# Kernel tuning notes

Measured on AMD Instinct MI355X. Metric: run time of the kernel, lower is better.

Reference implementation:

```python
import jax, jax.numpy as jnp
import numpy as np

N, H = 8192, 1024

def setup_inputs() -> dict:
    key = jax.random.key(0)
    ks = jax.random.split(key, 7)
    s = 1.0 / np.sqrt(H)
    return {
        "x": jax.random.normal(ks[0], (N, H), dtype=jnp.float32),
        "Wq": jax.random.uniform(ks[1], (H, H), dtype=jnp.float32, minval=-s, maxval=s),
        "bq": jax.random.uniform(ks[2], (H,), dtype=jnp.float32, minval=-s, maxval=s),
        "Wk": jax.random.uniform(ks[3], (H, H), dtype=jnp.float32, minval=-s, maxval=s),
        "bk": jax.random.uniform(ks[4], (H,), dtype=jnp.float32, minval=-s, maxval=s),
        "Wv": jax.random.uniform(ks[5], (H, H), dtype=jnp.float32, minval=-s, maxval=s),
        "bv": jax.random.uniform(ks[6], (H,), dtype=jnp.float32, minval=-s, maxval=s),
    }

def reference(x, Wq, bq, Wk, bk, Wv, bv):
    # q/k/v projections: [N, H]
    q = x @ Wq + bq
    k = x @ Wk + bk
    v = x @ Wv + bv
    # full scores [N, N]; NOTE: original has no 1/sqrt(d) scaling
    scores = q @ k.T
    alpha = jax.nn.softmax(scores, axis=1)
    return alpha @ v
```

## Files before the change

### kernel.cpp

```cpp
#include <hip/hip_runtime.h>
#include <hip/hip_bf16.h>
#include <hip/hip_fp16.h>


typedef _Float16 f16x8 __attribute__((ext_vector_type(8)));
typedef float floatx4 __attribute__((ext_vector_type(4)));
typedef float floatx2 __attribute__((ext_vector_type(2)));
typedef unsigned short ushortx8 __attribute__((ext_vector_type(8)));

__device__ __forceinline__ unsigned short f2h(float f) {
  __half h = __float2half(f);
  return __builtin_bit_cast(unsigned short, h);
}
__device__ __forceinline__ float h2f(unsigned short u) {
  return __half2float(__builtin_bit_cast(__half, u));
}

__device__ __forceinline__ void async16(const void* g, void* l) {
  __builtin_amdgcn_global_load_lds(
      (__attribute__((address_space(1))) unsigned int*)(g),
      (__attribute__((address_space(3))) unsigned int*)(l),
      16, 0, 0);
}


__global__ __launch_bounds__(256) void conv_f32_f16(const float* __restrict__ in,
                                                    unsigned short* __restrict__ out,
                                                    long n) {
  long i = ((long)blockIdx.x * 256 + threadIdx.x) * 4;
  if (i + 3 < n) {
    float4 f = *(const float4*)(in + i);
    ushort4 o;
    o.x = f2h(f.x); o.y = f2h(f.y); o.z = f2h(f.z); o.w = f2h(f.w);
    *(ushort4*)(out + i) = o;
  }
}

__global__ __launch_bounds__(256) void transpose_f32_f16_3(const float* __restrict__ in0,
                                                           const float* __restrict__ in1,
                                                           const float* __restrict__ in2,
                                                           unsigned short* __restrict__ out,
                                                           int rows, int cols) {
  const float* in = (blockIdx.z == 0) ? in0 : (blockIdx.z == 1) ? in1 : in2;
  unsigned short* o = out + (size_t)blockIdx.z * rows * cols;
  __shared__ float tile[32][33];
  int bx = blockIdx.x * 32;
  int by = blockIdx.y * 32;
  int tx = threadIdx.x & 31, ty = threadIdx.x >> 5;
  #pragma unroll
  for (int yy = ty; yy < 32; yy += 8)
    tile[yy][tx] = in[(size_t)(by + yy) * cols + bx + tx];
  __syncthreads();
  #pragma unroll
  for (int yy = ty; yy < 32; yy += 8)
    o[(size_t)(bx + yy) * rows + by + tx] = f2h(tile[tx][yy]);
}

template <int MODE>
__global__ __launch_bounds__(256, 4)
void gemm_bt(const unsigned short* __restrict__ A,
             const unsigned short* __restrict__ B,
             int M, int Nn, int K,
             const float* __restrict__ b0, const float* __restrict__ b1,
             const float* __restrict__ b2,
             unsigned short* __restrict__ out) {
  if constexpr (MODE == 0) {
    B   += (size_t)blockIdx.z * Nn * K;
    out += (size_t)blockIdx.z * M * Nn;
  }
  const float* bias = (MODE != 0) ? nullptr
                      : (blockIdx.z == 0) ? b0 : (blockIdx.z == 1) ? b1 : b2;
  __shared__ unsigned short smem[128 * 136];
  unsigned short* As = smem;
  unsigned short* Bs = smem + 128 * 32;
  const int tid  = threadIdx.x;
  const int wave = tid >> 6;
  const int lane = tid & 63;
  const int wm = wave >> 1, wn = wave & 1;
  const int quad = lane >> 4, l16 = lane & 15;
  const long bm = (long)blockIdx.y * 128;
  const long bn = (long)blockIdx.x * 128;

  floatx4 acc[4][4] = {};

  const int srow = wave * 32 + (lane >> 2);
  const int scol = (lane & 3) * 8;
  const unsigned short* gA0 = A + (bm + srow) * (long)K + scol;
  const unsigned short* gA1 = gA0 + 16L * K;
  const unsigned short* gB0 = B + (bn + srow) * (long)K + scol;
  const unsigned short* gB1 = gB0 + 16L * K;
  unsigned short* lA0 = &As[(wave * 32) * 32];
  unsigned short* lA1 = &As[(wave * 32 + 16) * 32];
  unsigned short* lB0 = &Bs[(wave * 32) * 32];
  unsigned short* lB1 = &Bs[(wave * 32 + 16) * 32];

  for (int kk = 0; kk < K; kk += 32) {
    async16(gA0 + kk, lA0);
    async16(gA1 + kk, lA1);
    async16(gB0 + kk, lB0);
    async16(gB1 + kk, lB1);
    __syncthreads();
    f16x8 af[4], bfv[4];
    #pragma unroll
    for (int i = 0; i < 4; ++i) {
      af[i]  = *reinterpret_cast<const f16x8*>(&As[(wm * 64 + i * 16 + l16) * 32 + quad * 8]);
      bfv[i] = *reinterpret_cast<const f16x8*>(&Bs[(wn * 64 + i * 16 + l16) * 32 + quad * 8]);
    }
    #pragma unroll
    for (int i = 0; i < 4; ++i)
      #pragma unroll
      for (int j = 0; j < 4; ++j)
        acc[i][j] = __builtin_amdgcn_mfma_f32_16x16x32_f16(af[i], bfv[j], acc[i][j], 0, 0, 0);
    __syncthreads();
  }
  #pragma unroll
  for (int i = 0; i < 4; ++i) {
    const int row0 = wm * 64 + i * 16 + quad * 4;
    #pragma unroll
    for (int j = 0; j < 4; ++j) {
      const int col = wn * 64 + j * 16 + l16;
      const float cb = (MODE == 0) ? bias[bn + col] : 0.0f;
      #pragma unroll
      for (int r = 0; r < 4; ++r)
        smem[(row0 + r) * 136 + col] = f2h(acc[i][j][r] + cb);
    }
  }
  __syncthreads();
  #pragma unroll
  for (int u = 0; u < 8; ++u) {
    const int chunk = u * 256 + tid;
    const int row = chunk >> 4;
    const int cc = chunk & 15;
    const ushortx8 val = *reinterpret_cast<const ushortx8*>(&smem[row * 136 + cc * 8]);
    *reinterpret_cast<ushortx8*>(&out[(bm + row) * (long)Nn + bn + cc * 8]) = val;
  }
}

__global__ __launch_bounds__(256) void softmax_compact(unsigned short* __restrict__ S,
                                                       int* __restrict__ nnz, int n) {
  const int row = blockIdx.x;
  const int tid = threadIdx.x;
  const int lane = tid & 63, w = tid >> 6;
  unsigned short* prow = S + (size_t)row * n;

  float v[32];
  float m = -1e30f;
  #pragma unroll
  for (int u = 0; u < 4; ++u) {
    const ushortx8 c = *reinterpret_cast<const ushortx8*>(&prow[tid * 32 + u * 8]);
    #pragma unroll
    for (int e = 0; e < 8; ++e) {
      v[u * 8 + e] = h2f(c[e]);
      m = fmaxf(m, v[u * 8 + e]);
    }
  }
  #pragma unroll
  for (int off = 32; off > 0; off >>= 1) m = fmaxf(m, __shfl_down(m, off, 64));
  __shared__ float redm[4];
  __shared__ int cnt;
  if (lane == 0) redm[w] = m;
  if (tid == 0) cnt = 0;
  __syncthreads();
  m = fmaxf(fmaxf(redm[0], redm[1]), fmaxf(redm[2], redm[3]));

  float s = 0.0f;
  #pragma unroll
  for (int i = 0; i < 32; ++i) {
    v[i] = __expf(v[i] - m);
    s += v[i];
  }
  #pragma unroll
  for (int off = 32; off > 0; off >>= 1) s += __shfl_down(s, off, 64);
  __shared__ float reds[4];
  if (lane == 0) reds[w] = s;
  __syncthreads();
  s = reds[0] + reds[1] + reds[2] + reds[3];
  const float inv = 1.0f / s;

  unsigned int* pairs = (unsigned int*)prow;
  const int cap = n / 2;
  #pragma unroll
  for (int i = 0; i < 32; ++i) {
    unsigned short hh = f2h(v[i] * inv);
    if (hh) {
      int p = atomicAdd(&cnt, 1);
      if (p < cap) pairs[p] = ((unsigned int)(tid * 32 + i) << 16) | hh;
    }
  }
  __syncthreads();
  const int c = (cnt < cap) ? cnt : cap;
  const int padded = (c + 7) & ~7;
  if (tid < padded - c) pairs[c + tid] = 0u;
  if (tid == 0) nnz[row] = padded;
}

__global__ __launch_bounds__(256) void pv_sliced(const unsigned short* __restrict__ S,
                                                 const int* __restrict__ nnz,
                                                 const unsigned short* __restrict__ v,
                                                 float* __restrict__ out,
                                                 int n) {
  const int wave = threadIdx.x >> 6;
  const int lane = threadIdx.x & 63;
  const int colbase = blockIdx.x * 128 + lane * 2;
  const unsigned colbyte = (unsigned)colbase * 2;
  const char* __restrict__ vb = (const char*)v;
  const char* __restrict__ sb = (const char*)S;

  #pragma unroll 1
  for (int r = 0; r < 4; ++r) {
    const int row = blockIdx.y + ((wave << 2) + r) * 512;
    int craw = nnz[row];
    craw = craw < 0 ? 0 : (craw > 4096 ? 4096 : craw);
    const int cnt = __builtin_amdgcn_readfirstlane(craw);
    const unsigned rowbase = (unsigned)row << 14;
    const unsigned pend = rowbase + 16384 - 32;
    unsigned poff = rowbase;
    uint4 q0 = *(const uint4*)(sb + poff);
    uint4 q1 = *(const uint4*)(sb + poff + 16);
    float a0 = 0.f, a1 = 0.f;
    for (int j = 0; j < cnt; j += 8) {
      const unsigned pn = (poff + 32 <= pend) ? poff + 32 : pend;
      const uint4 n0 = *(const uint4*)(sb + pn);
      const uint4 n1 = *(const uint4*)(sb + pn + 16);
      const unsigned p[8] = {q0.x, q0.y, q0.z, q0.w, q1.x, q1.y, q1.z, q1.w};
      #pragma unroll
      for (int u = 0; u < 8; ++u) {
        const ushort2 vv = *(const ushort2*)(vb + (((p[u] & 0xffff0000u) >> 5) + colbyte));
        const float w = h2f((unsigned short)(p[u] & 0xffffu));
        a0 += w * h2f(vv.x);
        a1 += w * h2f(vv.y);
      }
      q0 = n0; q1 = n1; poff = pn;
    }
    floatx2 o = {a0, a1};
    __builtin_nontemporal_store(o, (floatx2*)(out + ((size_t)row << 10) + colbase));
  }
}

extern "C" void kernel_launch(void* const* d_in, const int* in_sizes, int n_in,
                              void* d_out, int out_size, void* d_ws, size_t ws_size,
                              hipStream_t stream) {
  const int N = 8192, H = 1024;
  const float* x  = (const float*)d_in[0];
  const float* Wq = (const float*)d_in[1];
  const float* bq = (const float*)d_in[2];
  const float* Wk = (const float*)d_in[3];
  const float* bk = (const float*)d_in[4];
  const float* Wv = (const float*)d_in[5];
  const float* bv = (const float*)d_in[6];

  char* p = (char*)d_ws;
  unsigned short* xh  = (unsigned short*)p; p += (size_t)N * H * 2;
  unsigned short* WT  = (unsigned short*)p; p += (size_t)3 * H * H * 2;
  unsigned short* qkv = (unsigned short*)p; p += (size_t)3 * N * H * 2;
  unsigned short* S   = (unsigned short*)p; p += (size_t)N * N * 2;
  int*            nnz = (int*)p;            p += (size_t)N * 4;
  if ((size_t)(p - (char*)d_ws) > ws_size) return;
  unsigned short* qh = qkv;
  unsigned short* kh = qkv + (size_t)N * H;
  unsigned short* vh = qkv + (size_t)2 * N * H;

  conv_f32_f16<<<(N * H / 4 + 255) / 256, 256, 0, stream>>>(x, xh, (long)N * H);
  transpose_f32_f16_3<<<dim3(H / 32, H / 32, 3), 256, 0, stream>>>(Wq, Wk, Wv, WT, H, H);

  gemm_bt<0><<<dim3(H / 128, N / 128, 3), 256, 0, stream>>>(xh, WT, N, H, H,
                                                            bq, bk, bv, qkv);

  gemm_bt<1><<<dim3(N / 128, N / 128), 256, 0, stream>>>(qh, kh, N, N, H,
                                                         nullptr, nullptr, nullptr, S);
  softmax_compact<<<N, 256, 0, stream>>>(S, nnz, N);
  pv_sliced<<<dim3(8, N / 16), 256, 0, stream>>>(S, nnz, vh, (float*)d_out, N);
}
```

Baseline: 542.0 us.

## Assign one wave per softmax row and compact with ballot instead of atomics

The softmax-compaction kernel now gives each 64-lane wave a full row rather than a 256-thread block, which removes the shared-memory reductions and block barriers. The per-element LDS atomicAdd used to compact nonzero probabilities is replaced by a wave ballot plus popcount prefix, giving deterministic ordered output. It recomputes exp in the compaction pass instead of keeping the values, and holds 128 halves per lane in registers. The row length is hardcoded to 8192 and the capacity changes slightly.

After: 542.9 us. Within noise of the previous version (+0.2%).

```diff
diff --git a/kernel.cpp b/kernel.cpp
--- a/kernel.cpp
+++ b/kernel.cpp
@@ -138,60 +138,64 @@
 
 __global__ __launch_bounds__(256) void softmax_compact(unsigned short* __restrict__ S,
                                                        int* __restrict__ nnz, int n) {
-  const int row = blockIdx.x;
-  const int tid = threadIdx.x;
-  const int lane = tid & 63, w = tid >> 6;
-  unsigned short* prow = S + (size_t)row * n;
-
-  float v[32];
-  float m = -1e30f;
-  #pragma unroll
-  for (int u = 0; u < 4; ++u) {
-    const ushortx8 c = *reinterpret_cast<const ushortx8*>(&prow[tid * 32 + u * 8]);
+  const int wid  = threadIdx.x >> 6;
+  const int lane = threadIdx.x & 63;
+  const int row  = blockIdx.x * 4 + wid;
+  unsigned short* prow = S + ((size_t)row << 13);
+
+  ushortx8 c[16];
+  #pragma unroll
+  for (int u = 0; u < 16; ++u)
+    c[u] = *reinterpret_cast<const ushortx8*>(&prow[u * 512 + lane * 8]);
+
+  float m0 = -1e30f, m1 = -1e30f, m2 = -1e30f, m3 = -1e30f;
+  #pragma unroll
+  for (int u = 0; u < 16; ++u) {
+    m0 = fmaxf(m0, fmaxf(h2f(c[u][0]), h2f(c[u][4])));
+    m1 = fmaxf(m1, fmaxf(h2f(c[u][1]), h2f(c[u][5])));
+    m2 = fmaxf(m2, fmaxf(h2f(c[u][2]), h2f(c[u][6])));
+    m3 = fmaxf(m3, fmaxf(h2f(c[u][3]), h2f(c[u][7])));
+  }
+  float m = fmaxf(fmaxf(m0, m1), fmaxf(m2, m3));
+  #pragma unroll
+  for (int off = 32; off > 0; off >>= 1)
+    m = fmaxf(m, __shfl_xor(m, off, 64));
+
+  float s0 = 0.f, s1 = 0.f, s2 = 0.f, s3 = 0.f;
+  #pragma unroll
+  for (int u = 0; u < 16; ++u) {
+    s0 += __expf(h2f(c[u][0]) - m) + __expf(h2f(c[u][4]) - m);
+    s1 += __expf(h2f(c[u][1]) - m) + __expf(h2f(c[u][5]) - m);
+    s2 += __expf(h2f(c[u][2]) - m) + __expf(h2f(c[u][6]) - m);
+    s3 += __expf(h2f(c[u][3]) - m) + __expf(h2f(c[u][7]) - m);
+  }
+  float s = (s0 + s1) + (s2 + s3);
+  #pragma unroll
+  for (int off = 32; off > 0; off >>= 1)
+    s += __shfl_xor(s, off, 64);
+  const float inv = 1.0f / s;
+
+  unsigned int* pairs = (unsigned int*)prow;
+  const int cap = 4096 - 8;
+  int base = 0;
+  #pragma unroll
+  for (int u = 0; u < 16; ++u) {
     #pragma unroll
     for (int e = 0; e < 8; ++e) {
-      v[u * 8 + e] = h2f(c[e]);
-      m = fmaxf(m, v[u * 8 + e]);
-    }
-  }
-  #pragma unroll
-  for (int off = 32; off > 0; off >>= 1) m = fmaxf(m, __shfl_down(m, off, 64));
-  __shared__ float redm[4];
-  __shared__ int cnt;
-  if (lane == 0) redm[w] = m;
-  if (tid == 0) cnt = 0;
-  __syncthreads();
-  m = fmaxf(fmaxf(redm[0], redm[1]), fmaxf(redm[2], redm[3]));
-
-  float s = 0.0f;
-  #pragma unroll
-  for (int i = 0; i < 32; ++i) {
-    v[i] = __expf(v[i] - m);
-    s += v[i];
-  }
-  #pragma unroll
-  for (int off = 32; off > 0; off >>= 1) s += __shfl_down(s, off, 64);
-  __shared__ float reds[4];
-  if (lane == 0) reds[w] = s;
-  __syncthreads();
-  s = reds[0] + reds[1] + reds[2] + reds[3];
-  const float inv = 1.0f / s;
-
-  unsigned int* pairs = (unsigned int*)prow;
-  const int cap = n / 2;
-  #pragma unroll
-  for (int i = 0; i < 32; ++i) {
-    unsigned short hh = f2h(v[i] * inv);
-    if (hh) {
-      int p = atomicAdd(&cnt, 1);
-      if (p < cap) pairs[p] = ((unsigned int)(tid * 32 + i) << 16) | hh;
-    }
-  }
-  __syncthreads();
-  const int c = (cnt < cap) ? cnt : cap;
-  const int padded = (c + 7) & ~7;
-  if (tid < padded - c) pairs[c + tid] = 0u;
-  if (tid == 0) nnz[row] = padded;
+      const unsigned short hh = f2h(__expf(h2f(c[u][e]) - m) * inv);
+      const unsigned long long mask = __ballot(hh != 0);
+      if (hh) {
+        const int pos = base + (int)__popcll(mask & ((1ull << lane) - 1ull));
+        if (pos < cap)
+          pairs[pos] = ((unsigned)(u * 512 + lane * 8 + e) << 16) | hh;
+      }
+      base += (int)__popcll(mask);
+    }
+  }
+  const int c_cl = base < cap ? base : cap;
+  const int padded = (c_cl + 7) & ~7;
+  if (lane < padded - c_cl) pairs[c_cl + lane] = 0u;
+  if (lane == 0) nnz[row] = padded;
 }
 
 __global__ __launch_bounds__(256) void pv_sliced(const unsigned short* __restrict__ S,
@@ -268,6 +272,6 @@
 
   gemm_bt<1><<<dim3(N / 128, N / 128), 256, 0, stream>>>(qh, kh, N, N, H,
                                                          nullptr, nullptr, nullptr, S);
-  softmax_compact<<<N, 256, 0, stream>>>(S, nnz, N);
+  softmax_compact<<<N / 4, 256, 0, stream>>>(S, nnz, N);
   pv_sliced<<<dim3(8, N / 16), 256, 0, stream>>>(S, nnz, vh, (float*)d_out, N);
 }
```
